# Performance work log

Measured on AMD Instinct MI355X. Metric: run time of the kernel, lower is better.

The kernel has to match this reference:

```python
import jax, jax.numpy as jnp
import numpy as np

B, S, HID = 2, 2048, 4096
NH, NKV, HD = 32, 8, 128
N_REP = NH // NKV
SCALING = HD ** -0.5


def rotate_half(x):
    x1, x2 = x[..., : x.shape[-1] // 2], x[..., x.shape[-1] // 2 :]
    return jnp.concatenate((-x2, x1), axis=-1)


def setup_inputs() -> dict:
    key = jax.random.key(0)
    ks = jax.random.split(key, 8)
    hidden_states = jax.random.normal(ks[0], (B, S, HID), dtype=jnp.float32)
    # rotary embeddings (realistic cos/sin from inverse-frequency angles)
    inv_freq = 1.0 / (10000.0 ** (jnp.arange(0, HD, 2, dtype=jnp.float32) / HD))
    pos = jnp.arange(S, dtype=jnp.float32)
    ang = pos[:, None] * inv_freq[None, :]  # [S, HD/2]
    emb = jnp.concatenate([ang, ang], axis=-1)  # [S, HD]
    cos = jnp.broadcast_to(jnp.cos(emb)[None], (B, S, HD))
    sin = jnp.broadcast_to(jnp.sin(emb)[None], (B, S, HD))
    # additive causal mask [B,1,S,S]
    causal = jnp.triu(jnp.full((S, S), -1e9, dtype=jnp.float32), k=1)
    attention_mask = jnp.broadcast_to(causal[None, None], (B, 1, S, S))
    std = HID ** -0.5
    Wq = jax.random.normal(ks[1], (NH * HD, HID), dtype=jnp.float32) * std
    Wk = jax.random.normal(ks[2], (NKV * HD, HID), dtype=jnp.float32) * std
    Wv = jax.random.normal(ks[3], (NKV * HD, HID), dtype=jnp.float32) * std
    Wo = jax.random.normal(ks[4], (HID, NH * HD), dtype=jnp.float32) * std
    return {"hidden_states": hidden_states, "cos": cos, "sin": sin,
            "attention_mask": attention_mask, "Wq": Wq, "Wk": Wk, "Wv": Wv, "Wo": Wo}


def reference(hidden_states, cos, sin, attention_mask, Wq, Wk, Wv, Wo):
    b, s, _ = hidden_states.shape
    # projections (nn.Linear: x @ W.T), reshape to [B, H, S, D]
    q = (hidden_states @ Wq.T).reshape(b, s, NH, HD).transpose(0, 2, 1, 3)
    k = (hidden_states @ Wk.T).reshape(b, s, NKV, HD).transpose(0, 2, 1, 3)
    v = (hidden_states @ Wv.T).reshape(b, s, NKV, HD).transpose(0, 2, 1, 3)
    # RoPE, cos/sin broadcast over head dim
    c, sn = cos[:, None], sin[:, None]  # [B,1,S,D]
    q = q * c + rotate_half(q) * sn
    k = k * c + rotate_half(k) * sn
    # GQA repeat_kv
    k = jnp.repeat(k, N_REP, axis=1)
    v = jnp.repeat(v, N_REP, axis=1)
    # eager attention
    attn = jnp.einsum("bhqd,bhkd->bhqk", q, k) * SCALING
    attn = attn + attention_mask[:, :, :, : k.shape[2]]
    attn = jax.nn.softmax(attn.astype(jnp.float32), axis=-1).astype(q.dtype)
    out = jnp.einsum("bhqk,bhkd->bhqd", attn, v)
    out = out.transpose(0, 2, 1, 3).reshape(b, s, NH * HD)
    return out @ Wo.T
```

## Files before the change

### kernel.cpp

```cpp
#include <hip/hip_runtime.h>


typedef __bf16 bf16x8 __attribute__((ext_vector_type(8)));
typedef __bf16 bf16x4 __attribute__((ext_vector_type(4)));
typedef float floatx4 __attribute__((ext_vector_type(4)));

#define S_LEN 2048
#define HIDN  4096
#define NH    32
#define NKV   8
#define HD    128

__device__ inline void async_copy16(const void* g, void* l) {
  __builtin_amdgcn_global_load_lds(
      (const __attribute__((address_space(1))) void*)g,
      (__attribute__((address_space(3))) void*)l, 16, 0, 0);
}

template<int N> __device__ __forceinline__ void waitv() {
  static_assert(N == 0 || N == 6, "vmcnt");
  if constexpr (N == 0) asm volatile("s_waitcnt vmcnt(0)" ::: "memory");
  else                  asm volatile("s_waitcnt vmcnt(6)" ::: "memory");
}

__global__ __launch_bounds__(256) void cvt_bf16(const float* __restrict__ src,
                                                __bf16* __restrict__ dst, int n8)
{
  int i = blockIdx.x * 256 + threadIdx.x;
  if (i >= n8) return;
  const float4* s = (const float4*)src + (size_t)i * 2;
  float4 a = s[0], b = s[1];
  bf16x8 r = {(__bf16)a.x, (__bf16)a.y, (__bf16)a.z, (__bf16)a.w,
              (__bf16)b.x, (__bf16)b.y, (__bf16)b.z, (__bf16)b.w};
  *((bf16x8*)dst + i) = r;
}

__device__ __forceinline__ void gemm_core64(
    const __bf16* __restrict__ A, const __bf16* __restrict__ WB,
    __bf16* lds, int m0, int n0, int tid, floatx4 (&acc)[4][4])
{
  constexpr int A_BYTES = 128 * 64 * 2;
  constexpr int STAGE_B = (128 + 256) * 64 * 2;

  const int wave = tid >> 6, lane = tid & 63;
  const int quad = lane >> 4, l16 = lane & 15;
  const int wm = wave >> 2, wn = wave & 3;

  int a_off[2], b_off[4];
  #pragma unroll
  for (int ra = 0; ra < 2; ra++) {
    int idx = ra * 512 + tid;
    int row = idx >> 3, chunk = (idx & 7) ^ (row & 7);
    a_off[ra] = (m0 + row) * HIDN + chunk * 8;
  }
  #pragma unroll
  for (int rb = 0; rb < 4; rb++) {
    int idx = rb * 512 + tid;
    int row = idx >> 3, chunk = (idx & 7) ^ (row & 7);
    b_off[rb] = (n0 + row) * HIDN + chunk * 8;
  }

  const int swq  = (quad ^ (l16 & 3)) * 16;
  const int kxor = ((l16 >> 2) & 1) * 64;
  const int a_rd = (wm * 64 + l16) * 128 + swq;
  const int b_rd = A_BYTES + (wn * 64 + l16) * 128 + swq;

  #pragma unroll
  for (int mi = 0; mi < 4; mi++)
    #pragma unroll
    for (int ni = 0; ni < 4; ni++) acc[mi][ni] = (floatx4){0.f, 0.f, 0.f, 0.f};

  char* ldsb = (char*)lds;
  auto stage = [&](int kt, int slotB) {
    char* sb = ldsb + slotB;
    const size_t ko = (size_t)kt * 64;
    #pragma unroll
    for (int ra = 0; ra < 2; ra++)
      async_copy16(A + ko + a_off[ra], sb + (ra * 512 + tid) * 16);
    #pragma unroll
    for (int rb = 0; rb < 4; rb++)
      async_copy16(WB + ko + b_off[rb], sb + A_BYTES + (rb * 512 + tid) * 16);
  };
  auto read_frags = [&](int slotB, bf16x8 (&av)[4][2], bf16x8 (&bv)[4][2]) {
    const char* sb = ldsb + slotB;
    #pragma unroll
    for (int kk = 0; kk < 2; kk++) {
      const int kb = (kk << 6) ^ kxor;
      #pragma unroll
      for (int ni = 0; ni < 4; ni++)
        bv[ni][kk] = *(const bf16x8*)(sb + b_rd + ni * 2048 + kb);
      #pragma unroll
      for (int mi = 0; mi < 4; mi++)
        av[mi][kk] = *(const bf16x8*)(sb + a_rd + mi * 2048 + kb);
    }
  };
  auto mfma_tile = [&](bf16x8 (&av)[4][2], bf16x8 (&bv)[4][2]) {
    __builtin_amdgcn_s_setprio(1);
    #pragma unroll
    for (int kk = 0; kk < 2; kk++)
      #pragma unroll
      for (int mi = 0; mi < 4; mi++)
        #pragma unroll
        for (int ni = 0; ni < 4; ni++)
          acc[mi][ni] = __builtin_amdgcn_mfma_f32_16x16x32_bf16(
              bv[ni][kk], av[mi][kk], acc[mi][ni], 0, 0, 0);
    __builtin_amdgcn_s_setprio(0);
  };

  bf16x8 avA[4][2], bvA[4][2], avB[4][2], bvB[4][2];

  stage(0, 0);
  stage(1, STAGE_B);
  waitv<6>();
  __builtin_amdgcn_s_barrier();
  asm volatile("" ::: "memory");
  read_frags(0, avA, bvA);

  int oRead = STAGE_B, oStage = 2 * STAGE_B, oFree = 0;

#define GBODY(KT, AVc, BVc, AVn, BVn)                          \
  {                                                            \
    stage((KT) + 2, oStage);                                   \
    waitv<6>();                                                \
    asm volatile("s_waitcnt lgkmcnt(0)" ::: "memory");         \
    __builtin_amdgcn_s_barrier();                              \
    asm volatile("" ::: "memory");                             \
    read_frags(oRead, AVn, BVn);                               \
    mfma_tile(AVc, BVc);                                       \
    int t_ = oFree; oFree = oRead; oRead = oStage; oStage = t_;\
  }

  for (int kt = 0; kt < 62; kt += 2) {
    GBODY(kt,     avA, bvA, avB, bvB);
    GBODY(kt + 1, avB, bvB, avA, bvA);
  }
  {
    waitv<0>();
    asm volatile("s_waitcnt lgkmcnt(0)" ::: "memory");
    __builtin_amdgcn_s_barrier();
    asm volatile("" ::: "memory");
    read_frags(oRead, avB, bvB);
    mfma_tile(avA, bvA);
  }
  mfma_tile(avB, bvB);
#undef GBODY
}

__global__ __launch_bounds__(512, 2) void qkv_gemm_bf16(
    const __bf16* __restrict__ A, const __bf16* __restrict__ WB,
    __bf16* __restrict__ Qb, __bf16* __restrict__ Kb, __bf16* __restrict__ Vt)
{
  __shared__ __bf16 lds[3 * (128 + 256) * 32 * 2];
  const int tid = threadIdx.x;
  const int m0 = blockIdx.y * 128, n0 = blockIdx.x * 256;
  floatx4 acc[4][4];
  gemm_core64(A, WB, lds, m0, n0, tid, acc);

  const int wave = tid >> 6, lane = tid & 63;
  const int quad = lane >> 4, l16 = lane & 15;
  const int wm = wave >> 2, wn = wave & 3;
  #pragma unroll
  for (int mi = 0; mi < 4; mi++) {
    int m = m0 + wm * 64 + mi * 16 + l16;
    int b = m >> 11, s = m & (S_LEN - 1);
    #pragma unroll
    for (int ni = 0; ni < 4; ni++) {
      int nb = n0 + wn * 64 + ni * 16 + quad * 4;
      if (nb < 4096) {
        int hh = nb >> 7, d = nb & 127;
        bf16x4 v = {(__bf16)acc[mi][ni][0], (__bf16)acc[mi][ni][1],
                    (__bf16)acc[mi][ni][2], (__bf16)acc[mi][ni][3]};
        *(bf16x4*)&Qb[(((size_t)b * NH + hh) * S_LEN + s) * HD + d] = v;
      } else if (nb < 5120) {
        int nl = nb - 4096, hh = nl >> 7, d = nl & 127;
        bf16x4 v = {(__bf16)acc[mi][ni][0], (__bf16)acc[mi][ni][1],
                    (__bf16)acc[mi][ni][2], (__bf16)acc[mi][ni][3]};
        *(bf16x4*)&Kb[(((size_t)b * NKV + hh) * S_LEN + s) * HD + d] = v;
      } else {
        int nl = nb - 5120, hh = nl >> 7, d = nl & 127;
        #pragma unroll
        for (int r = 0; r < 4; r++)
          Vt[(((size_t)b * NKV + hh) * HD + d + r) * S_LEN + s] =
              (__bf16)acc[mi][ni][r];
      }
    }
  }
}

__global__ __launch_bounds__(512, 2) void out_gemm_bf16(
    const __bf16* __restrict__ A, const __bf16* __restrict__ WB,
    float* __restrict__ C)
{
  __shared__ __bf16 lds[3 * (128 + 256) * 32 * 2];
  const int tid = threadIdx.x;
  const int m0 = blockIdx.y * 128, n0 = blockIdx.x * 256;
  floatx4 acc[4][4];
  gemm_core64(A, WB, lds, m0, n0, tid, acc);

  const int wave = tid >> 6, lane = tid & 63;
  const int quad = lane >> 4, l16 = lane & 15;
  const int wm = wave >> 2, wn = wave & 3;
  #pragma unroll
  for (int mi = 0; mi < 4; mi++) {
    int m = m0 + wm * 64 + mi * 16 + l16;
    #pragma unroll
    for (int ni = 0; ni < 4; ni++) {
      int nb = n0 + wn * 64 + ni * 16 + quad * 4;
      *(floatx4*)&C[(size_t)m * HIDN + nb] = acc[mi][ni];
    }
  }
}

__global__ __launch_bounds__(256) void qkv_gemm_f32(
    const float* __restrict__ A, const float* __restrict__ Wq,
    const float* __restrict__ Wk, const float* __restrict__ Wv,
    __bf16* __restrict__ Qb, __bf16* __restrict__ Kb, __bf16* __restrict__ Vt)
{
  __shared__ __bf16 As[128 * 40];
  __shared__ __bf16 Bs[128 * 40];
  const int tid  = threadIdx.x;
  const int wave = tid >> 6, lane = tid & 63;
  const int quad = lane >> 4, l16 = lane & 15;
  const int wrow = (wave >> 1) * 64, wcol = (wave & 1) * 64;
  const int m0 = blockIdx.y * 128;
  const int n0 = blockIdx.x * 128;

  const float* W; int wr0; int sel;
  if (n0 < 4096)      { W = Wq; wr0 = n0;        sel = 0; }
  else if (n0 < 5120) { W = Wk; wr0 = n0 - 4096; sel = 1; }
  else                { W = Wv; wr0 = n0 - 5120; sel = 2; }

  floatx4 acc[4][4];
  #pragma unroll
  for (int i = 0; i < 4; i++)
    #pragma unroll
    for (int j = 0; j < 4; j++) acc[i][j] = (floatx4){0.f, 0.f, 0.f, 0.f};

  for (int k0 = 0; k0 < HIDN; k0 += 32) {
    __syncthreads();
    #pragma unroll
    for (int it = 0; it < 4; ++it) {
      int c = tid + it * 256;
      int row = c >> 3, c4 = (c & 7) * 4;
      float4 va = *(const float4*)(A + (size_t)(m0 + row) * HIDN + k0 + c4);
      __bf16* da = &As[row * 40 + c4];
      da[0] = (__bf16)va.x; da[1] = (__bf16)va.y; da[2] = (__bf16)va.z; da[3] = (__bf16)va.w;
      float4 vb = *(const float4*)(W + (size_t)(wr0 + row) * HIDN + k0 + c4);
      __bf16* db = &Bs[row * 40 + c4];
      db[0] = (__bf16)vb.x; db[1] = (__bf16)vb.y; db[2] = (__bf16)vb.z; db[3] = (__bf16)vb.w;
    }
    __syncthreads();
    bf16x8 af[4], bfr[4];
    #pragma unroll
    for (int i = 0; i < 4; i++)
      af[i] = *(const bf16x8*)&As[(wrow + i * 16 + l16) * 40 + quad * 8];
    #pragma unroll
    for (int j = 0; j < 4; j++)
      bfr[j] = *(const bf16x8*)&Bs[(wcol + j * 16 + l16) * 40 + quad * 8];
    #pragma unroll
    for (int i = 0; i < 4; i++)
      #pragma unroll
      for (int j = 0; j < 4; j++)
        acc[i][j] = __builtin_amdgcn_mfma_f32_16x16x32_bf16(af[i], bfr[j], acc[i][j], 0, 0, 0);
  }

  #pragma unroll
  for (int i = 0; i < 4; i++) {
    #pragma unroll
    for (int j = 0; j < 4; j++) {
      #pragma unroll
      for (int r = 0; r < 4; r++) {
        int m = m0 + wrow + i * 16 + quad * 4 + r;
        int n = n0 + wcol + j * 16 + l16;
        __bf16 v = (__bf16)acc[i][j][r];
        int b = m >> 11, s = m & (S_LEN - 1);
        if (sel == 0) {
          int h = n >> 7, d = n & 127;
          Qb[(((size_t)b * NH + h) * S_LEN + s) * HD + d] = v;
        } else if (sel == 1) {
          int nl = n - 4096, h = nl >> 7, d = nl & 127;
          Kb[(((size_t)b * NKV + h) * S_LEN + s) * HD + d] = v;
        } else {
          int nl = n - 5120, h = nl >> 7, d = nl & 127;
          Vt[(((size_t)b * NKV + h) * HD + d) * S_LEN + s] = v;
        }
      }
    }
  }
}

__global__ __launch_bounds__(256) void out_gemm_f32(
    const __bf16* __restrict__ A, const float* __restrict__ Wo,
    float* __restrict__ C)
{
  __shared__ __bf16 As[128 * 40];
  __shared__ __bf16 Bs[128 * 40];
  const int tid  = threadIdx.x;
  const int wave = tid >> 6, lane = tid & 63;
  const int quad = lane >> 4, l16 = lane & 15;
  const int wrow = (wave >> 1) * 64, wcol = (wave & 1) * 64;
  const int m0 = blockIdx.y * 128;
  const int n0 = blockIdx.x * 128;

  floatx4 acc[4][4];
  #pragma unroll
  for (int i = 0; i < 4; i++)
    #pragma unroll
    for (int j = 0; j < 4; j++) acc[i][j] = (floatx4){0.f, 0.f, 0.f, 0.f};

  for (int k0 = 0; k0 < HIDN; k0 += 32) {
    __syncthreads();
    #pragma unroll
    for (int it = 0; it < 2; ++it) {
      int c = tid + it * 256;
      int row = c >> 2, c8 = (c & 3) * 8;
      *(bf16x8*)&As[row * 40 + c8] =
          *(const bf16x8*)(A + (size_t)(m0 + row) * HIDN + k0 + c8);
    }
    #pragma unroll
    for (int it = 0; it < 4; ++it) {
      int c = tid + it * 256;
      int row = c >> 3, c4 = (c & 7) * 4;
      float4 vb = *(const float4*)(Wo + (size_t)(n0 + row) * HIDN + k0 + c4);
      __bf16* db = &Bs[row * 40 + c4];
      db[0] = (__bf16)vb.x; db[1] = (__bf16)vb.y; db[2] = (__bf16)vb.z; db[3] = (__bf16)vb.w;
    }
    __syncthreads();
    bf16x8 af[4], bfr[4];
    #pragma unroll
    for (int i = 0; i < 4; i++)
      af[i] = *(const bf16x8*)&As[(wrow + i * 16 + l16) * 40 + quad * 8];
    #pragma unroll
    for (int j = 0; j < 4; j++)
      bfr[j] = *(const bf16x8*)&Bs[(wcol + j * 16 + l16) * 40 + quad * 8];
    #pragma unroll
    for (int i = 0; i < 4; i++)
      #pragma unroll
      for (int j = 0; j < 4; j++)
        acc[i][j] = __builtin_amdgcn_mfma_f32_16x16x32_bf16(af[i], bfr[j], acc[i][j], 0, 0, 0);
  }

  #pragma unroll
  for (int i = 0; i < 4; i++)
    #pragma unroll
    for (int j = 0; j < 4; j++)
      #pragma unroll
      for (int r = 0; r < 4; r++) {
        int m = m0 + wrow + i * 16 + quad * 4 + r;
        int n = n0 + wcol + j * 16 + l16;
        C[(size_t)m * HIDN + n] = acc[i][j][r];
      }
}

__global__ __launch_bounds__(256) void rope_kernel(
    __bf16* __restrict__ Qb, __bf16* __restrict__ Kb,
    const float* __restrict__ cosp, const float* __restrict__ sinp)
{
  size_t i = (size_t)blockIdx.x * 256 + threadIdx.x;
  const size_t QP = (size_t)2 * NH * S_LEN * 8;
  __bf16* buf; int H; size_t t;
  if (i < QP) { buf = Qb; H = NH;  t = i; }
  else        { buf = Kb; H = NKV; t = i - QP; }
  int d0 = (int)(t & 7) * 8;
  int s  = (int)((t >> 3) & (S_LEN - 1));
  size_t rest = t >> 14;
  int h = (int)(rest % H);
  int b = (int)(rest / H);
  size_t base = (((size_t)b * H + h) * S_LEN + s) * HD;
  bf16x8 q0 = *(const bf16x8*)&buf[base + d0];
  bf16x8 q1 = *(const bf16x8*)&buf[base + d0 + 64];
  size_t cbase = ((size_t)b * S_LEN + s) * HD + d0;
  float4 c0 = *(const float4*)&cosp[cbase];
  float4 c1 = *(const float4*)&cosp[cbase + 4];
  float4 s0 = *(const float4*)&sinp[cbase];
  float4 s1 = *(const float4*)&sinp[cbase + 4];
  float cc[8] = {c0.x, c0.y, c0.z, c0.w, c1.x, c1.y, c1.z, c1.w};
  float ss[8] = {s0.x, s0.y, s0.z, s0.w, s1.x, s1.y, s1.z, s1.w};
  bf16x8 r0, r1;
  #pragma unroll
  for (int u = 0; u < 8; u++) {
    float a  = (float)q0[u];
    float bq = (float)q1[u];
    r0[u] = (__bf16)(a * cc[u] - bq * ss[u]);
    r1[u] = (__bf16)(bq * cc[u] + a * ss[u]);
  }
  *(bf16x8*)&buf[base + d0]      = r0;
  *(bf16x8*)&buf[base + d0 + 64] = r1;
}

__global__ __launch_bounds__(256, 2) void flash_attn(
    const __bf16* __restrict__ Q, const __bf16* __restrict__ Kc,
    const __bf16* __restrict__ Vt, __bf16* __restrict__ Out)
{
  __shared__ __bf16 Ks[64 * 136];
  __shared__ __bf16 VTs[128 * 72];
  __shared__ __bf16 Ps[4 * 32 * 72];
  const int tid  = threadIdx.x;
  const int wave = tid >> 6, lane = tid & 63;
  const int quad = lane >> 4, l16 = lane & 15;
  const int bh = blockIdx.x;
  const int h = bh & 31, b = bh >> 5;
  const int qt = 15 - (int)blockIdx.y;
  const int kvh = h >> 2;
  const size_t qbase  = (((size_t)b * NH + h) * S_LEN + qt * 128 + wave * 32) * HD;
  const size_t kbase  = ((size_t)b * NKV + kvh) * S_LEN * HD;
  const size_t vtbase = ((size_t)b * NKV + kvh) * (size_t)HD * S_LEN;
  const int psbase = wave * (32 * 72);

  bf16x8 qf[2][4];
  #pragma unroll
  for (int st = 0; st < 2; st++)
    #pragma unroll
    for (int kk = 0; kk < 4; kk++)
      qf[st][kk] = *(const bf16x8*)&Q[qbase + (size_t)(st * 16 + l16) * HD + kk * 32 + quad * 8];

  floatx4 o[2][8];
  floatx4 ol[2];
  #pragma unroll
  for (int st = 0; st < 2; st++) {
    ol[st] = (floatx4){0.f, 0.f, 0.f, 0.f};
    #pragma unroll
    for (int ct = 0; ct < 8; ct++) o[st][ct] = (floatx4){0.f, 0.f, 0.f, 0.f};
  }
  bf16x8 onesv;
  #pragma unroll
  for (int u = 0; u < 8; u++) onesv[u] = (__bf16)1.0f;

  const float c1 = 0.12753785f;
  const float c2 = -28.853900f;
  const int kj_end = 2 * qt + 2;

  bf16x8 kreg[4], vreg[4];
  #pragma unroll
  for (int it = 0; it < 4; ++it) {
    int c = tid + it * 256;
    kreg[it] = *(const bf16x8*)&Kc[kbase + (size_t)((c >> 4)) * HD + (c & 15) * 8];
    vreg[it] = *(const bf16x8*)&Vt[vtbase + (size_t)(c >> 3) * S_LEN + (c & 7) * 8];
  }

  for (int kj = 0; kj < kj_end; ++kj) {
    __syncthreads();
    #pragma unroll
    for (int it = 0; it < 4; ++it) {
      int c = tid + it * 256;
      *(bf16x8*)&Ks[(c >> 4) * 136 + (c & 15) * 8] = kreg[it];
      *(bf16x8*)&VTs[(c >> 3) * 72 + (c & 7) * 8] = vreg[it];
    }
    __syncthreads();

    if (kj + 1 < kj_end) {
      #pragma unroll
      for (int it = 0; it < 4; ++it) {
        int c = tid + it * 256;
        kreg[it] = *(const bf16x8*)&Kc[kbase + (size_t)((kj + 1) * 64 + (c >> 4)) * HD + (c & 15) * 8];
        vreg[it] = *(const bf16x8*)&Vt[vtbase + (size_t)(c >> 3) * S_LEN + (kj + 1) * 64 + (c & 7) * 8];
      }
    }

    floatx4 s[2][4];
    #pragma unroll
    for (int st = 0; st < 2; st++)
      #pragma unroll
      for (int j = 0; j < 4; j++) s[st][j] = (floatx4){0.f, 0.f, 0.f, 0.f};
    #pragma unroll
    for (int kk = 0; kk < 4; kk++) {
      bf16x8 ak[4];
      #pragma unroll
      for (int j = 0; j < 4; j++)
        ak[j] = *(const bf16x8*)&Ks[(j * 16 + l16) * 136 + kk * 32 + quad * 8];
      __builtin_amdgcn_s_setprio(1);
      #pragma unroll
      for (int st = 0; st < 2; st++)
        #pragma unroll
        for (int j = 0; j < 4; j++)
          s[st][j] = __builtin_amdgcn_mfma_f32_16x16x32_bf16(ak[j], qf[st][kk], s[st][j], 0, 0, 0);
      __builtin_amdgcn_s_setprio(0);
    }

    #pragma unroll
    for (int st = 0; st < 2; st++) {
      const int qrow = qt * 128 + wave * 32 + st * 16 + l16;
      #pragma unroll
      for (int j = 0; j < 4; j++) {
        const int kvb = kj * 64 + j * 16 + quad * 4;
        bf16x4 pw;
        #pragma unroll
        for (int r = 0; r < 4; r++) {
          float p = __builtin_amdgcn_exp2f(fmaf(s[st][j][r], c1, c2));
          if (kvb + r > qrow) p = 0.0f;
          pw[r] = (__bf16)p;
        }
        *(bf16x4*)&Ps[psbase + (st * 16 + l16) * 72 + j * 16 + quad * 4] = pw;
      }
    }

    #pragma unroll
    for (int kk = 0; kk < 2; kk++) {
      bf16x8 bv[8];
      #pragma unroll
      for (int ct = 0; ct < 8; ct++)
        bv[ct] = *(const bf16x8*)&VTs[(ct * 16 + l16) * 72 + kk * 32 + quad * 8];
      bf16x8 ap[2];
      #pragma unroll
      for (int st = 0; st < 2; st++)
        ap[st] = *(const bf16x8*)&Ps[psbase + (st * 16 + l16) * 72 + kk * 32 + quad * 8];
      __builtin_amdgcn_s_setprio(1);
      #pragma unroll
      for (int st = 0; st < 2; st++) {
        ol[st] = __builtin_amdgcn_mfma_f32_16x16x32_bf16(ap[st], onesv, ol[st], 0, 0, 0);
        #pragma unroll
        for (int ct = 0; ct < 8; ct++)
          o[st][ct] = __builtin_amdgcn_mfma_f32_16x16x32_bf16(ap[st], bv[ct], o[st][ct], 0, 0, 0);
      }
      __builtin_amdgcn_s_setprio(0);
    }
  }

  #pragma unroll
  for (int st = 0; st < 2; st++) {
    #pragma unroll
    for (int r = 0; r < 4; r++) {
      float rl = 1.0f / ol[st][r];
      int qi = qt * 128 + wave * 32 + st * 16 + quad * 4 + r;
      #pragma unroll
      for (int ct = 0; ct < 8; ct++) {
        Out[((size_t)b * S_LEN + qi) * HIDN + h * HD + ct * 16 + l16] =
            (__bf16)(o[st][ct][r] * rl);
      }
    }
  }
}

extern "C" void kernel_launch(void* const* d_in, const int* in_sizes, int n_in,
                              void* d_out, int out_size, void* d_ws, size_t ws_size,
                              hipStream_t stream)
{
  const float* hs   = (const float*)d_in[0];
  const float* cosp = (const float*)d_in[1];
  const float* sinp = (const float*)d_in[2];
  const float* Wq   = (const float*)d_in[4];
  const float* Wk   = (const float*)d_in[5];
  const float* Wv   = (const float*)d_in[6];
  const float* Wo   = (const float*)d_in[7];
  float* out = (float*)d_out;

  __bf16* Qb  = (__bf16*)d_ws;
  __bf16* Kb  = Qb  + (size_t)16777216;
  __bf16* Vtb = Kb  + (size_t)4194304;

  if (ws_size >= (size_t)134217728) {
    __bf16* HSB = Vtb + (size_t)4194304;
    __bf16* AO  = HSB;
    __bf16* WB  = HSB + (size_t)16777216;

    cvt_bf16<<<8192, 256, 0, stream>>>(hs, HSB, 2097152);
    cvt_bf16<<<8192, 256, 0, stream>>>(Wq, WB, 2097152);
    cvt_bf16<<<2048, 256, 0, stream>>>(Wk, WB + 16777216, 524288);
    cvt_bf16<<<2048, 256, 0, stream>>>(Wv, WB + 20971520, 524288);
    qkv_gemm_bf16<<<dim3(24, 32), 512, 0, stream>>>(HSB, WB, Qb, Kb, Vtb);
    cvt_bf16<<<8192, 256, 0, stream>>>(Wo, WB, 2097152);
    rope_kernel<<<5120, 256, 0, stream>>>(Qb, Kb, cosp, sinp);
    flash_attn<<<dim3(64, 16), 256, 0, stream>>>(Qb, Kb, Vtb, AO);
    out_gemm_bf16<<<dim3(16, 32), 512, 0, stream>>>(AO, WB, out);
  } else {
    __bf16* AO = Vtb + (size_t)4194304;
    qkv_gemm_f32<<<dim3(48, 32), 256, 0, stream>>>(hs, Wq, Wk, Wv, Qb, Kb, Vtb);
    rope_kernel<<<5120, 256, 0, stream>>>(Qb, Kb, cosp, sinp);
    flash_attn<<<dim3(64, 16), 256, 0, stream>>>(Qb, Kb, Vtb, AO);
    out_gemm_f32<<<dim3(32, 32), 256, 0, stream>>>(AO, Wo, out);
  }
}
```

Measured before the change: 672.9 us.

## Double-buffer K/V tiles via async global-to-LDS loads with XOR swizzle

The flash-attention loop stops staging K and V tiles through registers and writing them to LDS between two block barriers. Each tile now goes straight from global memory into LDS with asynchronous copies into two alternating buffers, so loading the next tile overlaps the current tile's MFMA work and each iteration needs only one barrier. The padded LDS rows are replaced by XOR-swizzled layouts for K, V^T and P to avoid bank conflicts without padding. The cost is more LDS per block (double buffers) and manual vmcnt/lgkmcnt waits that must stay matched to the number of copies in flight.

```diff
diff --git a/kernel.cpp b/kernel.cpp
--- a/kernel.cpp
+++ b/kernel.cpp
@@ -18,9 +18,10 @@
 }
 
 template<int N> __device__ __forceinline__ void waitv() {
-  static_assert(N == 0 || N == 6, "vmcnt");
-  if constexpr (N == 0) asm volatile("s_waitcnt vmcnt(0)" ::: "memory");
-  else                  asm volatile("s_waitcnt vmcnt(6)" ::: "memory");
+  static_assert(N == 0 || N == 6 || N == 8, "vmcnt");
+  if constexpr (N == 0)      asm volatile("s_waitcnt vmcnt(0)" ::: "memory");
+  else if constexpr (N == 6) asm volatile("s_waitcnt vmcnt(6)" ::: "memory");
+  else                       asm volatile("s_waitcnt vmcnt(8)" ::: "memory");
 }
 
 __global__ __launch_bounds__(256) void cvt_bf16(const float* __restrict__ src,
@@ -392,9 +393,9 @@
     const __bf16* __restrict__ Q, const __bf16* __restrict__ Kc,
     const __bf16* __restrict__ Vt, __bf16* __restrict__ Out)
 {
-  __shared__ __bf16 Ks[64 * 136];
-  __shared__ __bf16 VTs[128 * 72];
-  __shared__ __bf16 Ps[4 * 32 * 72];
+  __shared__ __bf16 Ks2[2][64 * 128];
+  __shared__ __bf16 VTs2[2][128 * 64];
+  __shared__ __bf16 Ps[4 * 32 * 64];
   const int tid  = threadIdx.x;
   const int wave = tid >> 6, lane = tid & 63;
   const int quad = lane >> 4, l16 = lane & 15;
@@ -405,7 +406,29 @@
   const size_t qbase  = (((size_t)b * NH + h) * S_LEN + qt * 128 + wave * 32) * HD;
   const size_t kbase  = ((size_t)b * NKV + kvh) * S_LEN * HD;
   const size_t vtbase = ((size_t)b * NKV + kvh) * (size_t)HD * S_LEN;
-  const int psbase = wave * (32 * 72);
+  const int psbase = wave * (32 * 64);
+
+  int ksrc[4], vsrc[4];
+  #pragma unroll
+  for (int it = 0; it < 4; ++it) {
+    int idx = it * 256 + tid;
+    { int r = idx >> 4, cs = idx & 15, cg = cs ^ (r & 15);
+      ksrc[it] = r * HD + cg * 8; }
+    { int r = idx >> 3, cs = idx & 7, cg = cs ^ (r & 7);
+      vsrc[it] = r * S_LEN + cg * 8; }
+  }
+  auto stageKV = [&](int kj, int slot) {
+    const __bf16* kp = Kc + kbase + (size_t)kj * 64 * HD;
+    const __bf16* vp = Vt + vtbase + (size_t)kj * 64;
+    char* kd = (char*)&Ks2[slot][0];
+    char* vd = (char*)&VTs2[slot][0];
+    #pragma unroll
+    for (int it = 0; it < 4; ++it) {
+      int dst = (it * 256 + tid) * 16;
+      async_copy16(kp + ksrc[it], kd + dst);
+      async_copy16(vp + vsrc[it], vd + dst);
+    }
+  };
 
   bf16x8 qf[2][4];
   #pragma unroll
@@ -430,32 +453,20 @@
   const float c2 = -28.853900f;
   const int kj_end = 2 * qt + 2;
 
-  bf16x8 kreg[4], vreg[4];
-  #pragma unroll
-  for (int it = 0; it < 4; ++it) {
-    int c = tid + it * 256;
-    kreg[it] = *(const bf16x8*)&Kc[kbase + (size_t)((c >> 4)) * HD + (c & 15) * 8];
-    vreg[it] = *(const bf16x8*)&Vt[vtbase + (size_t)(c >> 3) * S_LEN + (c & 7) * 8];
-  }
+  stageKV(0, 0);
+  stageKV(1, 1);
 
   for (int kj = 0; kj < kj_end; ++kj) {
-    __syncthreads();
-    #pragma unroll
-    for (int it = 0; it < 4; ++it) {
-      int c = tid + it * 256;
-      *(bf16x8*)&Ks[(c >> 4) * 136 + (c & 15) * 8] = kreg[it];
-      *(bf16x8*)&VTs[(c >> 3) * 72 + (c & 7) * 8] = vreg[it];
-    }
-    __syncthreads();
-
-    if (kj + 1 < kj_end) {
-      #pragma unroll
-      for (int it = 0; it < 4; ++it) {
-        int c = tid + it * 256;
-        kreg[it] = *(const bf16x8*)&Kc[kbase + (size_t)((kj + 1) * 64 + (c >> 4)) * HD + (c & 15) * 8];
-        vreg[it] = *(const bf16x8*)&Vt[vtbase + (size_t)(c >> 3) * S_LEN + (kj + 1) * 64 + (c & 7) * 8];
-      }
-    }
+    const int slot = kj & 1;
+    if (kj == 0) waitv<8>();
+    else         waitv<0>();
+    asm volatile("s_waitcnt lgkmcnt(0)" ::: "memory");
+    __builtin_amdgcn_s_barrier();
+    asm volatile("" ::: "memory");
+    if (kj >= 1 && kj + 1 < kj_end) stageKV(kj + 1, (kj + 1) & 1);
+
+    const __bf16* Ksl = &Ks2[slot][0];
+    const __bf16* Vsl = &VTs2[slot][0];
 
     floatx4 s[2][4];
     #pragma unroll
@@ -467,7 +478,7 @@
       bf16x8 ak[4];
       #pragma unroll
       for (int j = 0; j < 4; j++)
-        ak[j] = *(const bf16x8*)&Ks[(j * 16 + l16) * 136 + kk * 32 + quad * 8];
+        ak[j] = *(const bf16x8*)&Ksl[(j * 16 + l16) * 128 + (((kk * 4 + quad) ^ l16) * 8)];
       __builtin_amdgcn_s_setprio(1);
       #pragma unroll
       for (int st = 0; st < 2; st++)
@@ -490,7 +501,7 @@
           if (kvb + r > qrow) p = 0.0f;
           pw[r] = (__bf16)p;
         }
-        *(bf16x4*)&Ps[psbase + (st * 16 + l16) * 72 + j * 16 + quad * 4] = pw;
+        *(bf16x4*)&Ps[psbase + (st * 16 + l16) * 64 + (((j * 4 + quad) ^ (l16 & 14)) * 4)] = pw;
       }
     }
 
@@ -499,11 +510,11 @@
       bf16x8 bv[8];
       #pragma unroll
       for (int ct = 0; ct < 8; ct++)
-        bv[ct] = *(const bf16x8*)&VTs[(ct * 16 + l16) * 72 + kk * 32 + quad * 8];
+        bv[ct] = *(const bf16x8*)&Vsl[(ct * 16 + l16) * 64 + (((kk * 4 + quad) ^ (l16 & 7)) * 8)];
       bf16x8 ap[2];
       #pragma unroll
       for (int st = 0; st < 2; st++)
-        ap[st] = *(const bf16x8*)&Ps[psbase + (st * 16 + l16) * 72 + kk * 32 + quad * 8];
+        ap[st] = *(const bf16x8*)&Ps[psbase + (st * 16 + l16) * 64 + (((kk * 8 + quad * 2) ^ (l16 & 14)) * 4)];
       __builtin_amdgcn_s_setprio(1);
       #pragma unroll
       for (int st = 0; st < 2; st++) {
```

Measured after the change: 666.9 us. About the same (-0.9%).
